# Performance work log

Measured on AMD Instinct MI355X. Metric: run time of the kernel, lower is better.

Reference implementation:

```python
import jax, jax.numpy as jnp
import numpy as np

# Constants from init_kwargs
DT = 0.01
NIV = 8          # energy_input_dim[1]
HID = 64         # hidden_dims[0]
FEAT = 501       # per-field microstructure feature length (501+501=1002)


def _lin(k, fin, fout):
    return jax.random.normal(k, (fin, fout), dtype=jnp.float32) / np.sqrt(fin)


def setup_inputs() -> dict:
    key = jax.random.key(0)
    ks = jax.random.split(key, 12)
    B, T = 8192, 512
    e = jax.random.normal(ks[0], (B, T, 1), dtype=jnp.float32) * 0.1
    e_dot = jax.random.normal(ks[1], (B, T, 1), dtype=jnp.float32) * 0.1
    # positive microstructure fields (code computes nu**-1 and E/nu**2)
    E = jax.random.uniform(ks[2], (B, FEAT), minval=0.5, maxval=2.0, dtype=jnp.float32)
    nu = jax.random.uniform(ks[3], (B, FEAT), minval=0.5, maxval=2.0, dtype=jnp.float32)
    return {
        "e": e, "e_dot": e_dot, "E": E, "nu": nu,
        # EnergyFunction.B : Linear(1002,64) -> ReLU -> Linear(64,niv)
        "Bw1": _lin(ks[4], 2 * FEAT, HID), "Bb1": jnp.zeros((HID,), jnp.float32),
        "Bw2": _lin(ks[5], HID, NIV), "Bb2": jnp.zeros((NIV,), jnp.float32),
        # InverseDissipationPotential.beta : Linear(1002,64)->Softplus->Linear(64,niv)->Softplus
        "bw1": _lin(ks[6], 2 * FEAT, HID), "bb1": jnp.zeros((HID,), jnp.float32),
        "bw2": _lin(ks[7], HID, NIV), "bb2": jnp.zeros((NIV,), jnp.float32),
    }


def reference(e, e_dot, E, nu, Bw1, Bb1, Bw2, Bb2, bw1, bb1, bw2, bb2):
    # --- microstructure encoder (TrueFeatures) ---
    nu_p = 1.0 / jnp.mean(1.0 / nu, axis=1, keepdims=True)                 # [B,1]
    E_p = jnp.mean(E / nu ** 2, axis=1, keepdims=True) * nu_p ** 2         # [B,1]
    m = jnp.concatenate([E, nu], axis=-1)                                  # [B,1002]

    # Time-invariant MLP coefficients (hoisted out of the time loop)
    Bm = jax.nn.relu(m @ Bw1 + Bb1) @ Bw2 + Bb2                            # [B,NIV]
    beta = jax.nn.softplus(jax.nn.softplus(m @ bw1 + bb1) @ bw2 + bb2)     # [B,NIV]
    Bsum = jnp.sum(Bm, axis=-1, keepdims=True)                             # [B,1]

    B_, niv = Bm.shape
    xi0 = jnp.zeros((B_, niv), dtype=e.dtype)

    def step(xi, inp):
        u, p = inp                                                          # [B,1],[B,1]
        # Analytic gradients of L = sum_{b,k} Bm_bk * (0.5*E' u^2 + 0.5*(u-xi_k)^2 + 0.5*sum_j xi_j^2)
        du = u - xi                                                         # [B,NIV]
        grad_u = Bsum * E_p * u + jnp.sum(Bm * du, axis=-1, keepdims=True)  # [B,1] (s_eq)
        grad_v = -Bm * du + Bsum * xi                                       # [B,NIV] (d)
        q = -grad_v
        # Analytic gradients of potential = -0.5*nu' p^2 + 0.5*sum(beta*q^2)
        grad_p = -nu_p * p                                                  # [B,1] (s_neq)
        grad_q = beta * q                                                   # [B,NIV] (kinetics)
        stress = grad_u - grad_p
        return xi + DT * grad_q, (stress, xi)

    xs = (jnp.swapaxes(e, 0, 1), jnp.swapaxes(e_dot, 0, 1))                 # [T,B,1]
    _, (stress_t, xi_t) = jax.lax.scan(step, xi0, xs)
    stress = jnp.swapaxes(stress_t, 0, 1)                                   # [B,T,1]
    xi = jnp.swapaxes(xi_t, 0, 1)                                           # [B,T,NIV]
    return stress, xi
```

## Files before the change

kernel.cpp:

```cpp
#include <hip/hip_runtime.h>
#include <hip/hip_bf16.h>

#define FEATN 501
#define KPAD 1024
#define NB 8192
#define NT 512
#define DTC 0.01f

typedef __attribute__((ext_vector_type(8))) short short8;
typedef __attribute__((ext_vector_type(4))) float f32x4;

__device__ __forceinline__ float softplus_f(float x) {
    return fmaxf(x, 0.f) + log1pf(expf(-fabsf(x)));
}
__device__ __forceinline__ ushort f2bf(float x) {
    __hip_bfloat16 h = __float2bfloat16(x);
    return *reinterpret_cast<ushort*>(&h);
}
__device__ __forceinline__ void gl_lds16(const void* g, void* l) {
    __builtin_amdgcn_global_load_lds(
        (const __attribute__((address_space(1))) void*)g,
        (__attribute__((address_space(3))) void*)l, 16, 0, 0);
}
__device__ __forceinline__ float dpp_add(float x, const int ctrl) {
    int s = __builtin_bit_cast(int, x);
    int y;
    switch (ctrl) {
    case 0xB1:  y = __builtin_amdgcn_update_dpp(0, s, 0xB1, 0xf, 0xf, true); break;
    case 0x4E:  y = __builtin_amdgcn_update_dpp(0, s, 0x4E, 0xf, 0xf, true); break;
    default:    y = __builtin_amdgcn_update_dpp(0, s, 0x141, 0xf, 0xf, true); break;
    }
    return x + __builtin_bit_cast(float, y);
}

__global__ __launch_bounds__(256) void prep_kernel(
    const float* __restrict__ E, const float* __restrict__ nu,
    float* __restrict__ out) {
    const int b = blockIdx.x * 4 + (threadIdx.x >> 6);
    const int lane = threadIdx.x & 63;
    const size_t base = (size_t)b * FEATN;
    float* cb = out + (size_t)NB * NT + (size_t)b * 4096;
    ushort* mb = (ushort*)(cb + 512);
    float s1 = 0.f, s2 = 0.f;
    for (int i = lane; i < FEATN; i += 64) {
        const float Ev = E[base + i];
        const float nv = nu[base + i];
        const float inv = 1.0f / nv;
        s1 += inv;
        s2 = fmaf(Ev, inv * inv, s2);
        mb[i] = f2bf(Ev);
        mb[FEATN + i] = f2bf(nv);
    }
    if (lane < KPAD - 2 * FEATN) mb[2 * FEATN + lane] = 0;
    #pragma unroll
    for (int o = 32; o; o >>= 1) { s1 += __shfl_xor(s1, o); s2 += __shfl_xor(s2, o); }
    if (lane == 0) {
        const float np = (float)FEATN / s1;
        cb[26] = np;
        cb[27] = (s2 / (float)FEATN) * np * np;
    }
}

__global__ __launch_bounds__(256) void wtrans_kernel(
    const float* __restrict__ Bw1, const float* __restrict__ bw1,
    ushort* __restrict__ Wt) {
    const int h = blockIdx.x;
    const int lane = threadIdx.x & 63;
    const int wv = threadIdx.x >> 6;
    const float* W = (h < 64) ? Bw1 : bw1;
    const int col = h & 63;
    #pragma unroll
    for (int it = 0; it < 4; ++it) {
        const int k = it * 256 + wv * 64 + lane;
        const float v = (k < 2 * FEATN) ? W[(size_t)k * 64 + col] : 0.f;
        Wt[(size_t)h * KPAD + k] = f2bf(v);
    }
}

__global__ __launch_bounds__(256) void enc_kernel(
    const ushort* __restrict__ Wt,
    const float* __restrict__ Bb1, const float* __restrict__ bb1,
    const float* __restrict__ Bw2, const float* __restrict__ Bb2,
    const float* __restrict__ bw2, const float* __restrict__ bb2,
    float* __restrict__ out) {
    __shared__ ushort Wl[2][4096];
    __shared__ ushort Ml[2][512];
    __shared__ float hid[128][17];
    const int tid = threadIdx.x;
    const int wv = tid >> 6, lane = tid & 63;
    const int bb0 = blockIdx.x * 16;
    float* xi = out + (size_t)NB * NT;

    const int srow = lane >> 2;
    const int sslot = lane & 3;
    const ushort* mbase = (const ushort*)(xi + (size_t)(bb0 + srow) * 4096 + 512);
    const int n0 = wv * 2;

    auto stage = [&](int s, int buf) {
        const int kb = s * 32;
        gl_lds16(Wt + (size_t)(n0 * 16 + srow) * KPAD + kb + sslot * 8,
                 &Wl[buf][n0 * 512]);
        gl_lds16(Wt + (size_t)(n0 * 16 + 16 + srow) * KPAD + kb + sslot * 8,
                 &Wl[buf][n0 * 512 + 512]);
        if (wv == 3) gl_lds16(mbase + kb + sslot * 8, &Ml[buf][0]);
    };

    const int r15 = lane & 15, kg = lane >> 4;
    const int aoff0 = (wv * 32 + r15) * 32 + kg * 8;
    const int aoff1 = aoff0 + 16 * 32;
    const int boff = r15 * 32 + kg * 8;

    f32x4 acc0 = {0.f, 0.f, 0.f, 0.f}, acc1 = acc0;
    stage(0, 0);
    __syncthreads();
    for (int s = 0; s < 32; ++s) {
        const int buf = s & 1;
        if (s + 1 < 32) stage(s + 1, buf ^ 1);
        short8 a0 = *(const short8*)&Wl[buf][aoff0];
        short8 a1 = *(const short8*)&Wl[buf][aoff1];
        short8 b = *(const short8*)&Ml[buf][boff];
        acc0 = __builtin_amdgcn_mfma_f32_16x16x32_bf16(a0, b, acc0, 0, 0, 0);
        acc1 = __builtin_amdgcn_mfma_f32_16x16x32_bf16(a1, b, acc1, 0, 0, 0);
        __syncthreads();
    }

    #pragma unroll
    for (int t = 0; t < 2; ++t) {
        #pragma unroll
        for (int r = 0; r < 4; ++r) {
            const int h = wv * 32 + t * 16 + kg * 4 + r;
            const float bias = (h < 64) ? Bb1[h] : bb1[h - 64];
            float v = (t ? acc1[r] : acc0[r]) + bias;
            v = (h < 64) ? fmaxf(v, 0.f) : softplus_f(v);
            hid[h][r15] = v;
        }
    }
    __syncthreads();

    if (tid < 128) {
        const int bl = tid >> 3, k = tid & 7;
        float dB = 0.f, db = 0.f;
        #pragma unroll 8
        for (int h = 0; h < 64; ++h) {
            dB = fmaf(hid[h][bl], Bw2[h * 8 + k], dB);
            db = fmaf(hid[64 + h][bl], bw2[h * 8 + k], db);
        }
        const float Bm = dB + Bb2[k];
        const float be = softplus_f(db + bb2[k]);
        float Bs = Bm;
        Bs += __shfl_xor(Bs, 1);
        Bs += __shfl_xor(Bs, 2);
        Bs += __shfl_xor(Bs, 4);
        float* cb = xi + (size_t)(bb0 + bl) * 4096;
        const float np = cb[26];
        const float Ep = cb[27];
        cb[k] = 1.f - DTC * be * (Bm + Bs);
        cb[8 + k] = DTC * be * Bm;
        cb[16 + k] = Bm;
        if (k == 0) { cb[24] = Bs * Ep; cb[25] = np; }
    }
}

__global__ __launch_bounds__(256) void time_kernel(
    const float* __restrict__ e, const float* __restrict__ ed,
    const float* coef, float* stress, float* xi_out) {
    __shared__ float els[4][512];
    __shared__ float pls[4][512];
    const int wv = threadIdx.x >> 6;
    const int wid = (blockIdx.x << 2) + wv;
    const int lane = threadIdx.x & 63;
    const int j = lane >> 3, k = lane & 7;

    const float* eb = e + (size_t)wid * NT;
    const float* edb = ed + (size_t)wid * NT;
    gl_lds16(eb + lane * 4, &els[wv][0]);
    gl_lds16(eb + 256 + lane * 4, &els[wv][256]);
    gl_lds16(edb + lane * 4, &pls[wv][0]);
    gl_lds16(edb + 256 + lane * 4, &pls[wv][256]);

    const float* cb = coef + (size_t)wid * 4096;
    const float a = cb[k];
    const float c = cb[8 + k];
    const float Bm = cb[16 + k];
    const float sE = cb[24];
    const float nup = cb[25];
    asm volatile("s_waitcnt vmcnt(0)" ::: "memory");

    const float a2 = a * a, a4 = a2 * a2;
    const float P = a4 * a4;
    float A = 1.f;
    if (j & 1) A *= a;
    if (j & 2) A *= a2;
    if (j & 4) A *= a4;
    float pw[8];
    {
        float run = c;
        #pragma unroll
        for (int i = 7; i >= 0; --i) {
            const bool on = (i < j);
            pw[i] = on ? run : 0.f;
            run = on ? run * a : run;
        }
    }
    float pv[8];
    pv[7] = c;
    #pragma unroll
    for (int i = 6; i >= 0; --i) pv[i] = a * pv[i + 1];

    float* xb = xi_out + (size_t)wid * (NT * 8);
    float* sb = stress + (size_t)wid * NT;
    const float* el = &els[wv][0];
    const float* pl = &pls[wv][0];

    float4 q0 = *(const float4*)(el);
    float4 q1 = *(const float4*)(el + 4);
    float uj = el[j];
    float pj = pl[j];

    float xs = 0.f;
    #pragma unroll 2
    for (int t0 = 0; t0 < NT; t0 += 8) {
        const float u0 = q0.x, u1 = q0.y, u2 = q0.z, u3 = q0.w;
        const float u4 = q1.x, u5 = q1.y, u6 = q1.z, u7 = q1.w;
        const float cuj = uj, cpj = pj;
        if (t0 + 8 < NT) {
            q0 = *(const float4*)(el + t0 + 8);
            q1 = *(const float4*)(el + t0 + 12);
            uj = el[t0 + 8 + j];
            pj = pl[t0 + 8 + j];
        }
        float xi_j = A * xs;
        xi_j = fmaf(pw[0], u0, xi_j);
        xi_j = fmaf(pw[1], u1, xi_j);
        xi_j = fmaf(pw[2], u2, xi_j);
        xi_j = fmaf(pw[3], u3, xi_j);
        xi_j = fmaf(pw[4], u4, xi_j);
        xi_j = fmaf(pw[5], u5, xi_j);
        xi_j = fmaf(pw[6], u6, xi_j);
        xi_j = fmaf(pw[7], u7, xi_j);
        float ns = P * xs;
        ns = fmaf(pv[0], u0, ns);
        ns = fmaf(pv[1], u1, ns);
        ns = fmaf(pv[2], u2, ns);
        ns = fmaf(pv[3], u3, ns);
        ns = fmaf(pv[4], u4, ns);
        ns = fmaf(pv[5], u5, ns);
        ns = fmaf(pv[6], u6, ns);
        ns = fmaf(pv[7], u7, ns);
        xs = ns;
        xb[t0 * 8 + lane] = xi_j;
        float r = Bm * (cuj - xi_j);
        r = dpp_add(r, 0xB1);
        r = dpp_add(r, 0x4E);
        r = dpp_add(r, 0x141);
        if (k == 0) sb[t0 + j] = fmaf(sE, cuj, fmaf(nup, cpj, r));
    }
}

extern "C" void kernel_launch(void* const* d_in, const int* in_sizes, int n_in,
                              void* d_out, int out_size, void* d_ws, size_t ws_size,
                              hipStream_t stream) {
    const float* e   = (const float*)d_in[0];
    const float* ed  = (const float*)d_in[1];
    const float* E   = (const float*)d_in[2];
    const float* nu  = (const float*)d_in[3];
    const float* Bw1 = (const float*)d_in[4];
    const float* Bb1 = (const float*)d_in[5];
    const float* Bw2 = (const float*)d_in[6];
    const float* Bb2 = (const float*)d_in[7];
    const float* bw1 = (const float*)d_in[8];
    const float* bb1 = (const float*)d_in[9];
    const float* bw2 = (const float*)d_in[10];
    const float* bb2 = (const float*)d_in[11];

    float* out = (float*)d_out;
    float* stress = out;
    float* xi = out + (size_t)NB * NT;
    ushort* Wt = (ushort*)out;

    prep_kernel<<<2048, 256, 0, stream>>>(E, nu, out);
    wtrans_kernel<<<128, 256, 0, stream>>>(Bw1, bw1, Wt);
    enc_kernel<<<512, 256, 0, stream>>>(Wt, Bb1, bb1, Bw2, Bb2, bw2, bb2, out);
    time_kernel<<<2048, 256, 0, stream>>>(e, ed, xi, stress, xi);
}
```

Measured before the change: 70.97 us.

## Fuse microstructure prep into encoder and read weights directly from global

Removes the separate prep kernel. The encoder block now loads E and nu itself, computes the nu_p and E_p reductions, and writes the bf16 features straight into a padded LDS tile. The round trip of features through global memory goes away, and the weight transpose is remapped to the new padded K layout. The double-buffered LDS staging of weights and its per-step barriers are replaced by direct global vector loads feeding MFMA. The time kernel's outputs now use nontemporal stores. Risks are unaligned float4 loads on odd-length rows and uncached weight reads repeated by every block.

```diff
diff --git a/kernel.cpp b/kernel.cpp
--- a/kernel.cpp
+++ b/kernel.cpp
@@ -3,11 +3,13 @@
 
 #define FEATN 501
 #define KPAD 1024
+#define MSTRIDE 1032
 #define NB 8192
 #define NT 512
 #define DTC 0.01f
 
 typedef __attribute__((ext_vector_type(8))) short short8;
+typedef __attribute__((ext_vector_type(4))) short short4v;
 typedef __attribute__((ext_vector_type(4))) float f32x4;
 
 __device__ __forceinline__ float softplus_f(float x) {
@@ -31,34 +33,6 @@
     default:    y = __builtin_amdgcn_update_dpp(0, s, 0x141, 0xf, 0xf, true); break;
     }
     return x + __builtin_bit_cast(float, y);
-}
-
-__global__ __launch_bounds__(256) void prep_kernel(
-    const float* __restrict__ E, const float* __restrict__ nu,
-    float* __restrict__ out) {
-    const int b = blockIdx.x * 4 + (threadIdx.x >> 6);
-    const int lane = threadIdx.x & 63;
-    const size_t base = (size_t)b * FEATN;
-    float* cb = out + (size_t)NB * NT + (size_t)b * 4096;
-    ushort* mb = (ushort*)(cb + 512);
-    float s1 = 0.f, s2 = 0.f;
-    for (int i = lane; i < FEATN; i += 64) {
-        const float Ev = E[base + i];
-        const float nv = nu[base + i];
-        const float inv = 1.0f / nv;
-        s1 += inv;
-        s2 = fmaf(Ev, inv * inv, s2);
-        mb[i] = f2bf(Ev);
-        mb[FEATN + i] = f2bf(nv);
-    }
-    if (lane < KPAD - 2 * FEATN) mb[2 * FEATN + lane] = 0;
-    #pragma unroll
-    for (int o = 32; o; o >>= 1) { s1 += __shfl_xor(s1, o); s2 += __shfl_xor(s2, o); }
-    if (lane == 0) {
-        const float np = (float)FEATN / s1;
-        cb[26] = np;
-        cb[27] = (s2 / (float)FEATN) * np * np;
-    }
 }
 
 __global__ __launch_bounds__(256) void wtrans_kernel(
@@ -72,56 +46,93 @@
     #pragma unroll
     for (int it = 0; it < 4; ++it) {
         const int k = it * 256 + wv * 64 + lane;
-        const float v = (k < 2 * FEATN) ? W[(size_t)k * 64 + col] : 0.f;
+        const int ksrc = (k < FEATN) ? k
+                       : (k >= 512 && k < 512 + FEATN) ? k - 11 : -1;
+        const float v = (ksrc >= 0) ? W[(size_t)ksrc * 64 + col] : 0.f;
         Wt[(size_t)h * KPAD + k] = f2bf(v);
     }
 }
 
 __global__ __launch_bounds__(256) void enc_kernel(
+    const float* __restrict__ E, const float* __restrict__ nu,
     const ushort* __restrict__ Wt,
     const float* __restrict__ Bb1, const float* __restrict__ bb1,
     const float* __restrict__ Bw2, const float* __restrict__ Bb2,
     const float* __restrict__ bw2, const float* __restrict__ bb2,
-    float* __restrict__ out) {
-    __shared__ ushort Wl[2][4096];
-    __shared__ ushort Ml[2][512];
+    float* __restrict__ xi) {
+    __shared__ ushort Ml[16 * MSTRIDE];
     __shared__ float hid[128][17];
+    __shared__ float nups[16], Eps[16];
+
     const int tid = threadIdx.x;
     const int wv = tid >> 6, lane = tid & 63;
     const int bb0 = blockIdx.x * 16;
-    float* xi = out + (size_t)NB * NT;
-
-    const int srow = lane >> 2;
-    const int sslot = lane & 3;
-    const ushort* mbase = (const ushort*)(xi + (size_t)(bb0 + srow) * 4096 + 512);
-    const int n0 = wv * 2;
-
-    auto stage = [&](int s, int buf) {
+
+    {
+        const int bl = tid >> 4;
+        const int t16 = tid & 15;
+        const size_t base = (size_t)(bb0 + bl) * FEATN;
+        float s1 = 0.f, s2 = 0.f;
+        #pragma unroll
+        for (int it = 0; it < 8; ++it) {
+            const int i0 = it * 64 + t16 * 4;
+            if (i0 + 3 < FEATN) {
+                const float4 Ev = *(const float4*)(E + base + i0);
+                const float4 nv = *(const float4*)(nu + base + i0);
+                const float i0v = 1.0f / nv.x, i1v = 1.0f / nv.y;
+                const float i2v = 1.0f / nv.z, i3v = 1.0f / nv.w;
+                s1 += (i0v + i1v) + (i2v + i3v);
+                s2 = fmaf(Ev.x, i0v * i0v, s2);
+                s2 = fmaf(Ev.y, i1v * i1v, s2);
+                s2 = fmaf(Ev.z, i2v * i2v, s2);
+                s2 = fmaf(Ev.w, i3v * i3v, s2);
+                short4v ep = {(short)f2bf(Ev.x), (short)f2bf(Ev.y),
+                              (short)f2bf(Ev.z), (short)f2bf(Ev.w)};
+                short4v np_ = {(short)f2bf(nv.x), (short)f2bf(nv.y),
+                               (short)f2bf(nv.z), (short)f2bf(nv.w)};
+                *(short4v*)&Ml[bl * MSTRIDE + i0] = ep;
+                *(short4v*)&Ml[bl * MSTRIDE + 512 + i0] = np_;
+            } else if (i0 < FEATN) {
+                const float Ev = E[base + i0];
+                const float nv = nu[base + i0];
+                const float iv = 1.0f / nv;
+                s1 += iv;
+                s2 = fmaf(Ev, iv * iv, s2);
+                Ml[bl * MSTRIDE + i0] = f2bf(Ev);
+                Ml[bl * MSTRIDE + 512 + i0] = f2bf(nv);
+            }
+        }
+        if (t16 < 11) {
+            Ml[bl * MSTRIDE + FEATN + t16] = 0;
+            Ml[bl * MSTRIDE + 512 + FEATN + t16] = 0;
+        }
+        #pragma unroll
+        for (int o = 1; o < 16; o <<= 1) {
+            s1 += __shfl_xor(s1, o);
+            s2 += __shfl_xor(s2, o);
+        }
+        if (t16 == 0) {
+            const float np = (float)FEATN / s1;
+            nups[bl] = np;
+            Eps[bl] = (s2 / (float)FEATN) * np * np;
+        }
+    }
+    __syncthreads();
+
+    const int r15 = lane & 15, kg = lane >> 4;
+    const ushort* wp0 = Wt + (size_t)(wv * 32 + r15) * KPAD + kg * 8;
+    const ushort* wp1 = wp0 + 16 * KPAD;
+    const int boff = r15 * MSTRIDE + kg * 8;
+
+    f32x4 acc0 = {0.f, 0.f, 0.f, 0.f}, acc1 = acc0;
+    #pragma unroll 4
+    for (int s = 0; s < 32; ++s) {
         const int kb = s * 32;
-        gl_lds16(Wt + (size_t)(n0 * 16 + srow) * KPAD + kb + sslot * 8,
-                 &Wl[buf][n0 * 512]);
-        gl_lds16(Wt + (size_t)(n0 * 16 + 16 + srow) * KPAD + kb + sslot * 8,
-                 &Wl[buf][n0 * 512 + 512]);
-        if (wv == 3) gl_lds16(mbase + kb + sslot * 8, &Ml[buf][0]);
-    };
-
-    const int r15 = lane & 15, kg = lane >> 4;
-    const int aoff0 = (wv * 32 + r15) * 32 + kg * 8;
-    const int aoff1 = aoff0 + 16 * 32;
-    const int boff = r15 * 32 + kg * 8;
-
-    f32x4 acc0 = {0.f, 0.f, 0.f, 0.f}, acc1 = acc0;
-    stage(0, 0);
-    __syncthreads();
-    for (int s = 0; s < 32; ++s) {
-        const int buf = s & 1;
-        if (s + 1 < 32) stage(s + 1, buf ^ 1);
-        short8 a0 = *(const short8*)&Wl[buf][aoff0];
-        short8 a1 = *(const short8*)&Wl[buf][aoff1];
-        short8 b = *(const short8*)&Ml[buf][boff];
+        const short8 a0 = *(const short8*)(wp0 + kb);
+        const short8 a1 = *(const short8*)(wp1 + kb);
+        const short8 b = *(const short8*)&Ml[boff + kb];
         acc0 = __builtin_amdgcn_mfma_f32_16x16x32_bf16(a0, b, acc0, 0, 0, 0);
         acc1 = __builtin_amdgcn_mfma_f32_16x16x32_bf16(a1, b, acc1, 0, 0, 0);
-        __syncthreads();
     }
 
     #pragma unroll
@@ -152,12 +163,10 @@
         Bs += __shfl_xor(Bs, 2);
         Bs += __shfl_xor(Bs, 4);
         float* cb = xi + (size_t)(bb0 + bl) * 4096;
-        const float np = cb[26];
-        const float Ep = cb[27];
         cb[k] = 1.f - DTC * be * (Bm + Bs);
         cb[8 + k] = DTC * be * Bm;
         cb[16 + k] = Bm;
-        if (k == 0) { cb[24] = Bs * Ep; cb[25] = np; }
+        if (k == 0) { cb[24] = Bs * Eps[bl]; cb[25] = nups[bl]; }
     }
 }
 
@@ -248,12 +257,14 @@
         ns = fmaf(pv[6], u6, ns);
         ns = fmaf(pv[7], u7, ns);
         xs = ns;
-        xb[t0 * 8 + lane] = xi_j;
+        __builtin_nontemporal_store(xi_j, &xb[t0 * 8 + lane]);
         float r = Bm * (cuj - xi_j);
         r = dpp_add(r, 0xB1);
         r = dpp_add(r, 0x4E);
         r = dpp_add(r, 0x141);
-        if (k == 0) sb[t0 + j] = fmaf(sE, cuj, fmaf(nup, cpj, r));
+        if (k == 0)
+            __builtin_nontemporal_store(fmaf(sE, cuj, fmaf(nup, cpj, r)),
+                                        &sb[t0 + j]);
     }
 }
 
@@ -278,8 +289,8 @@
     float* xi = out + (size_t)NB * NT;
     ushort* Wt = (ushort*)out;
 
-    prep_kernel<<<2048, 256, 0, stream>>>(E, nu, out);
     wtrans_kernel<<<128, 256, 0, stream>>>(Bw1, bw1, Wt);
-    enc_kernel<<<512, 256, 0, stream>>>(Wt, Bb1, bb1, Bw2, Bb2, bw2, bb2, out);
+    enc_kernel<<<512, 256, 0, stream>>>(E, nu, Wt, Bb1, bb1,
+                                        Bw2, Bb2, bw2, bb2, xi);
     time_kernel<<<2048, 256, 0, stream>>>(e, ed, xi, stress, xi);
 }
```

After: 85.80 us. 20.9% more time.
